# Optimization experiments

Measured on AMD Instinct MI355X. Metric: run time of the kernel, lower is better.

The kernel has to match this reference:

```python
import jax, jax.numpy as jnp
import numpy as np

B, C, H, W = 8, 256, 128, 128
CQ = C // 8


def setup_inputs() -> dict:
    key = jax.random.key(0)
    ks = jax.random.split(key, 8)
    s = 1.0 / np.sqrt(C)
    return {
        "x": jax.random.normal(ks[0], (B, C, H, W), dtype=jnp.float32),
        "wq": jax.random.normal(ks[1], (CQ, C), dtype=jnp.float32) * s,
        "bq": jax.random.normal(ks[2], (CQ,), dtype=jnp.float32) * 0.01,
        "wk": jax.random.normal(ks[3], (CQ, C), dtype=jnp.float32) * s,
        "bk": jax.random.normal(ks[4], (CQ,), dtype=jnp.float32) * 0.01,
        "wv": jax.random.normal(ks[5], (C, C), dtype=jnp.float32) * s,
        "bv": jax.random.normal(ks[6], (C,), dtype=jnp.float32) * 0.01,
        "gamma": jax.random.normal(ks[7], (1,), dtype=jnp.float32) * 0.1,
    }


def reference(x, wq, bq, wk, bk, wv, bv, gamma):
    b, c, h, w = x.shape
    # 1x1 convs == channel matmuls
    q = jnp.einsum("oc,bchw->bohw", wq, x) + bq[None, :, None, None]  # [B,Cq,H,W]
    k = jnp.einsum("oc,bchw->bohw", wk, x) + bk[None, :, None, None]  # [B,Cq,H,W]
    v = jnp.einsum("oc,bchw->bohw", wv, x) + bv[None, :, None, None]  # [B,C,H,W]

    # column (height) scores: energy_H[b,i,w,j] = <k[:, i, w], q[:, j, w]>, -inf on i==j
    e_h = jnp.einsum("bciw,bcjw->biwj", k, q)  # [B,H,W,H]
    diag = jnp.eye(h, dtype=bool)[:, None, :]  # [H,1,H] -> masks i==j
    e_h = jnp.where(diag[None], -jnp.inf, e_h)

    # row (width) scores: energy_W[b,h,i,j] = <k[:, h, i], q[:, h, j]>
    e_w = jnp.einsum("bchi,bchj->bhij", k, q)  # [B,H,W,W]

    # joint softmax over concatenated H+W scores (axis 3), as in the torch code
    att = jax.nn.softmax(jnp.concatenate([e_h, e_w], axis=3), axis=3)
    a_h, a_w = att[..., :h], att[..., h:]

    out_h = jnp.einsum("bciw,biwj->bcjw", v, a_h)  # aggregate along column
    out_w = jnp.einsum("bchi,bhij->bchj", v, a_w)  # aggregate along row
    return gamma * (out_h + out_w) + x
```

## Files before the change

kernel.cpp:

```cpp
#include <hip/hip_runtime.h>
#include <math.h>

#define C_   256
#define CQ_  32
#define H_   128
#define W_   128
#define HW_  (H_ * W_)
#define OC_  320

typedef __attribute__((ext_vector_type(8))) short  s8v;
typedef __attribute__((ext_vector_type(4))) float  f4v;
typedef __attribute__((ext_vector_type(8))) unsigned short u8v;
typedef __attribute__((ext_vector_type(4))) unsigned short u4v;

__device__ inline unsigned short f2bf(float f) {
    unsigned int u = __float_as_uint(f);
    unsigned int r = (u + 0x7fffu + ((u >> 16) & 1u)) >> 16;
    return (unsigned short)r;
}
__device__ inline float bfu(unsigned short u) {
    return __uint_as_float((unsigned int)u << 16);
}

__global__ __launch_bounds__(256) void k_wconv(
    const float* __restrict__ wq, const float* __restrict__ wk,
    const float* __restrict__ wv, unsigned short* __restrict__ Wb)
{
    int idx4 = blockIdx.x * 256 + threadIdx.x;
    int e = idx4 * 4;
    int oc = e >> 8, k = e & 255;
    const float* src;
    if (oc < 32)      src = wq + (size_t)oc * C_ + k;
    else if (oc < 64) src = wk + (size_t)(oc - 32) * C_ + k;
    else              src = wv + (size_t)(oc - 64) * C_ + k;
    float4 v = *(const float4*)src;
    u4v o;
    o[0] = f2bf(v.x); o[1] = f2bf(v.y); o[2] = f2bf(v.z); o[3] = f2bf(v.w);
    *(u4v*)(Wb + e) = o;
}

__global__ __launch_bounds__(256) void k_qkv(
    const float* __restrict__ x, const unsigned short* __restrict__ Wb,
    const float* __restrict__ bq, const float* __restrict__ bk,
    const float* __restrict__ bv,
    unsigned short* __restrict__ qkv, int b0)
{
    __shared__ __align__(16) unsigned short Wl[2][64][72];
    __shared__ __align__(16) unsigned int   Xp[2][32 * 132];
    const int t = threadIdx.x;
    const int lane = t & 63;
    const int wave = t >> 6;
    const int n0 = blockIdx.x * 128;
    const int ocblk = blockIdx.y * 64;
    const int bb = blockIdx.z;
    const float* xb = x + (size_t)(b0 + bb) * C_ * HW_;

    const int lg = lane >> 4;
    const int ll = lane & 15;
    const int n_w = wave * 32;

    const int kp8 = t >> 5;
    const int n4  = (t & 31) * 4;
    const int wrow = t >> 3;
    const int wcg  = (t & 7) * 8;
    float4 ra[4], rb[4];
    u8v wreg[2];

    #pragma unroll
    for (int p = 0; p < 4; ++p) {
        int krow = (p * 8 + kp8) * 2;
        ra[p] = *(const float4*)(xb + (size_t)krow * HW_ + n0 + n4);
        rb[p] = *(const float4*)(xb + (size_t)(krow + 1) * HW_ + n0 + n4);
    }
    #pragma unroll
    for (int q = 0; q < 2; ++q)
        wreg[q] = *(const u8v*)(Wb + (size_t)(ocblk + wrow + q * 32) * C_ + wcg);

    #pragma unroll
    for (int p = 0; p < 4; ++p) {
        uint4 d;
        const float* af  = (const float*)&ra[p];
        const float* bf_ = (const float*)&rb[p];
        #pragma unroll
        for (int i = 0; i < 4; ++i) {
            unsigned int lo = (__float_as_uint(af[i])  + 0x8000u) >> 16;
            unsigned int hi = (__float_as_uint(bf_[i]) + 0x8000u) & 0xffff0000u;
            ((unsigned int*)&d)[i] = hi | lo;
        }
        *(uint4*)&Xp[0][(p * 8 + kp8) * 132 + n4] = d;
    }
    #pragma unroll
    for (int q = 0; q < 2; ++q)
        *(u8v*)&Wl[0][wrow + q * 32][wcg] = wreg[q];

    #pragma unroll
    for (int p = 0; p < 4; ++p) {
        int krow = 64 + (p * 8 + kp8) * 2;
        ra[p] = *(const float4*)(xb + (size_t)krow * HW_ + n0 + n4);
        rb[p] = *(const float4*)(xb + (size_t)(krow + 1) * HW_ + n0 + n4);
    }
    #pragma unroll
    for (int q = 0; q < 2; ++q)
        wreg[q] = *(const u8v*)(Wb + (size_t)(ocblk + wrow + q * 32) * C_ + 64 + wcg);

    f4v acc[4][2];
    #pragma unroll
    for (int mr = 0; mr < 4; ++mr)
        #pragma unroll
        for (int nr = 0; nr < 2; ++nr)
            acc[mr][nr] = (f4v){0.f, 0.f, 0.f, 0.f};

    __syncthreads();

    #pragma unroll
    for (int kc = 0; kc < 4; ++kc) {
        const int cur = kc & 1;
        if (kc < 3) {
            #pragma unroll
            for (int p = 0; p < 4; ++p) {
                uint4 d;
                const float* af  = (const float*)&ra[p];
                const float* bf_ = (const float*)&rb[p];
                #pragma unroll
                for (int i = 0; i < 4; ++i) {
                    unsigned int lo = (__float_as_uint(af[i])  + 0x8000u) >> 16;
                    unsigned int hi = (__float_as_uint(bf_[i]) + 0x8000u) & 0xffff0000u;
                    ((unsigned int*)&d)[i] = hi | lo;
                }
                *(uint4*)&Xp[cur ^ 1][(p * 8 + kp8) * 132 + n4] = d;
            }
            #pragma unroll
            for (int q = 0; q < 2; ++q)
                *(u8v*)&Wl[cur ^ 1][wrow + q * 32][wcg] = wreg[q];
        }
        if (kc < 2) {
            #pragma unroll
            for (int p = 0; p < 4; ++p) {
                int krow = (kc + 2) * 64 + (p * 8 + kp8) * 2;
                ra[p] = *(const float4*)(xb + (size_t)krow * HW_ + n0 + n4);
                rb[p] = *(const float4*)(xb + (size_t)(krow + 1) * HW_ + n0 + n4);
            }
            #pragma unroll
            for (int q = 0; q < 2; ++q)
                wreg[q] = *(const u8v*)(
                    Wb + (size_t)(ocblk + wrow + q * 32) * C_ + (kc + 2) * 64 + wcg);
        }
        #pragma unroll
        for (int ks = 0; ks < 2; ++ks) {
            s8v afr[4];
            #pragma unroll
            for (int mr = 0; mr < 4; ++mr)
                afr[mr] = *(const s8v*)&Wl[cur][mr * 16 + ll][ks * 32 + lg * 8];
            #pragma unroll
            for (int nr = 0; nr < 2; ++nr) {
                int4 bd;
                #pragma unroll
                for (int e2 = 0; e2 < 4; ++e2)
                    ((int*)&bd)[e2] =
                        Xp[cur][(ks * 16 + lg * 4 + e2) * 132 + n_w + nr * 16 + ll];
                s8v bfr = *(s8v*)&bd;
                #pragma unroll
                for (int mr = 0; mr < 4; ++mr)
                    acc[mr][nr] = __builtin_amdgcn_mfma_f32_16x16x32_bf16(
                        afr[mr], bfr, acc[mr][nr], 0, 0, 0);
            }
        }
        __syncthreads();
    }

    #pragma unroll
    for (int mr = 0; mr < 4; ++mr) {
        float bias[4];
        #pragma unroll
        for (int r = 0; r < 4; ++r) {
            int oc = ocblk + mr * 16 + lg * 4 + r;
            if (oc < 32)      bias[r] = bq[oc];
            else if (oc < 64) bias[r] = bk[oc - 32];
            else              bias[r] = bv[oc - 64];
        }
        #pragma unroll
        for (int nr = 0; nr < 2; ++nr) {
            int n = n0 + n_w + nr * 16 + ll;
            #pragma unroll
            for (int r = 0; r < 4; ++r) {
                int oc = ocblk + mr * 16 + lg * 4 + r;
                qkv[((size_t)bb * OC_ + oc) * HW_ + n] = f2bf(acc[mr][nr][r] + bias[r]);
            }
        }
    }
}

__global__ __launch_bounds__(256) void k_transpose_qkv(
    const unsigned short* __restrict__ qkv, unsigned short* __restrict__ qkv_t)
{
    __shared__ unsigned short tile[32][34];
    const int bb = blockIdx.z;
    const int oc = blockIdx.y;
    const int th = (blockIdx.x & 3) * 32;
    const int tw = (blockIdx.x >> 2) * 32;
    const unsigned short* src = qkv + ((size_t)bb * OC_ + oc) * HW_;
    #pragma unroll
    for (int r = 0; r < 4; ++r) {
        int h = threadIdx.y * 4 + r;
        tile[h][threadIdx.x] = src[(size_t)(th + h) * W_ + tw + threadIdx.x];
    }
    __syncthreads();
    unsigned short* dst = qkv_t + (size_t)bb * W_ * OC_ * H_;
    #pragma unroll
    for (int r = 0; r < 4; ++r) {
        int wl = threadIdx.y * 4 + r;
        dst[((size_t)(tw + wl) * OC_ + oc) * H_ + th + threadIdx.x] = tile[threadIdx.x][wl];
    }
}

__device__ inline void stage_KQ(const unsigned short* base, int cstride,
                                unsigned int* Ktp, unsigned int* Qp, int t)
{
    {
        int i = t & 127, half = t >> 7, c0 = half * 16;
        unsigned int kr[16];
        #pragma unroll
        for (int cc = 0; cc < 16; ++cc)
            kr[cc] = base[(size_t)(32 + c0 + cc) * cstride + i];
        uint4 d0, d1;
        #pragma unroll
        for (int e2 = 0; e2 < 4; ++e2)
            ((unsigned int*)&d0)[e2] = kr[2 * e2] | (kr[2 * e2 + 1] << 16);
        #pragma unroll
        for (int e2 = 0; e2 < 4; ++e2)
            ((unsigned int*)&d1)[e2] = kr[8 + 2 * e2] | (kr[9 + 2 * e2] << 16);
        *(uint4*)&Ktp[i * 20 + half * 8]     = d0;
        *(uint4*)&Ktp[i * 20 + half * 8 + 4] = d1;
    }
    {
        int c2 = t >> 4, j8 = (t & 15) * 8;
        u8v qa = *(const u8v*)(base + (size_t)(2 * c2) * cstride + j8);
        u8v qb = *(const u8v*)(base + (size_t)(2 * c2 + 1) * cstride + j8);
        uint4 e0, e1;
        #pragma unroll
        for (int e = 0; e < 4; ++e)
            ((unsigned int*)&e0)[e] =
                (unsigned int)qa[e] | ((unsigned int)qb[e] << 16);
        #pragma unroll
        for (int e = 0; e < 4; ++e)
            ((unsigned int*)&e1)[e] =
                (unsigned int)qa[4 + e] | ((unsigned int)qb[4 + e] << 16);
        *(uint4*)&Qp[c2 * 132 + j8]     = e0;
        *(uint4*)&Qp[c2 * 132 + j8 + 4] = e1;
    }
}

__device__ inline f4v eqk_mfma(const unsigned int* Ktp, const unsigned int* Qp,
                               int mr, int j, int lg, int ll)
{
    s8v afr = *(const s8v*)&Ktp[(mr * 16 + ll) * 20 + lg * 4];
    int4 bd;
    #pragma unroll
    for (int e2 = 0; e2 < 4; ++e2)
        ((int*)&bd)[e2] = Qp[(lg * 4 + e2) * 132 + j];
    s8v bfr = *(s8v*)&bd;
    return __builtin_amdgcn_mfma_f32_16x16x32_bf16(
        afr, bfr, (f4v){0.f, 0.f, 0.f, 0.f}, 0, 0, 0);
}

__global__ __launch_bounds__(256) void k_stats_h(
    const unsigned short* __restrict__ qkv_t,
    float* __restrict__ mh, float* __restrict__ sh)
{
    __shared__ __align__(16) unsigned int Ktp[128 * 20];
    __shared__ __align__(16) unsigned int Qp[16 * 132];
    const int t = threadIdx.x;
    const int beta = blockIdx.x;
    const int bb = blockIdx.y;
    const unsigned short* base = qkv_t + ((size_t)bb * W_ + beta) * OC_ * H_;
    stage_KQ(base, H_, Ktp, Qp, t);
    __syncthreads();

    const int lane = t & 63;
    const int wv = t >> 6;
    const int lg = lane >> 4;
    const int ll = lane & 15;

    #pragma unroll
    for (int ml = 0; ml < 2; ++ml) {
        const int mr = wv * 2 + ml;
        const int i0 = mr * 16 + lg * 4;
        f4v ef[8];
        #pragma unroll
        for (int nt = 0; nt < 8; ++nt) {
            f4v e = eqk_mfma(Ktp, Qp, mr, nt * 16 + ll, lg, ll);
            int j = nt * 16 + ll;
            #pragma unroll
            for (int r = 0; r < 4; ++r)
                if (i0 + r == j) e[r] = -INFINITY;
            ef[nt] = e;
        }
        #pragma unroll
        for (int r = 0; r < 4; ++r) {
            float mm = -INFINITY;
            #pragma unroll
            for (int nt = 0; nt < 8; ++nt) mm = fmaxf(mm, ef[nt][r]);
            #pragma unroll
            for (int s = 1; s < 16; s <<= 1) mm = fmaxf(mm, __shfl_xor(mm, s));
            float ss = 0.f;
            #pragma unroll
            for (int nt = 0; nt < 8; ++nt) ss += __expf(ef[nt][r] - mm);
            #pragma unroll
            for (int s = 1; s < 16; s <<= 1) ss += __shfl_xor(ss, s);
            if (ll == 0) {
                int i = i0 + r;
                mh[((size_t)bb * H_ + i) * W_ + beta] = mm;
                sh[((size_t)bb * H_ + i) * W_ + beta] = ss;
            }
        }
    }
}

__global__ __launch_bounds__(256) void k_stats_w(
    const unsigned short* __restrict__ qkv,
    float* __restrict__ mw, float* __restrict__ sw)
{
    __shared__ __align__(16) unsigned int Ktp[128 * 20];
    __shared__ __align__(16) unsigned int Qp[16 * 132];
    const int t = threadIdx.x;
    const int alpha = blockIdx.x;
    const int bb = blockIdx.y;
    const unsigned short* base = qkv + (size_t)bb * OC_ * HW_ + (size_t)alpha * W_;
    stage_KQ(base, HW_, Ktp, Qp, t);
    __syncthreads();

    const int lane = t & 63;
    const int wv = t >> 6;
    const int lg = lane >> 4;
    const int ll = lane & 15;

    #pragma unroll
    for (int ml = 0; ml < 2; ++ml) {
        const int mr = wv * 2 + ml;
        const int i0 = mr * 16 + lg * 4;
        f4v ef[8];
        #pragma unroll
        for (int nt = 0; nt < 8; ++nt)
            ef[nt] = eqk_mfma(Ktp, Qp, mr, nt * 16 + ll, lg, ll);
        #pragma unroll
        for (int r = 0; r < 4; ++r) {
            float mm = -INFINITY;
            #pragma unroll
            for (int nt = 0; nt < 8; ++nt) mm = fmaxf(mm, ef[nt][r]);
            #pragma unroll
            for (int s = 1; s < 16; s <<= 1) mm = fmaxf(mm, __shfl_xor(mm, s));
            float ss = 0.f;
            #pragma unroll
            for (int nt = 0; nt < 8; ++nt) ss += __expf(ef[nt][r] - mm);
            #pragma unroll
            for (int s = 1; s < 16; s <<= 1) ss += __shfl_xor(ss, s);
            if (ll == 0) {
                int i = i0 + r;
                mw[((size_t)bb * H_ + alpha) * W_ + i] = mm;
                sw[((size_t)bb * H_ + alpha) * W_ + i] = ss;
            }
        }
    }
}

__global__ __launch_bounds__(256) void k_prep(
    const float* __restrict__ mh, const float* __restrict__ sh,
    const float* __restrict__ mw, const float* __restrict__ sw,
    float* __restrict__ mc, float* __restrict__ dv,
    float* __restrict__ mct, float* __restrict__ dvt, int n)
{
    int idx = blockIdx.x * 256 + threadIdx.x;
    if (idx >= n) return;
    float m1 = mh[idx], s1 = sh[idx], m2 = mw[idx], s2 = sw[idx];
    float m = fmaxf(m1, m2);
    float d = 1.f / (s1 * __expf(m1 - m) + s2 * __expf(m2 - m));
    mc[idx] = m; dv[idx] = d;
    int q = idx & (W_ - 1);
    int p = (idx >> 7) & (H_ - 1);
    int b = idx >> 14;
    size_t tid = ((size_t)b * W_ + q) * H_ + p;
    mct[tid] = m; dvt[tid] = d;
}

__global__ __launch_bounds__(256) void k_outh(
    const unsigned short* __restrict__ qkv_t,
    const float* __restrict__ mct, const float* __restrict__ dvt,
    unsigned short* __restrict__ oh_t)
{
    __shared__ __align__(16) unsigned short Pt[128 * 128];
    __shared__ __align__(16) unsigned char  Ubuf[18688];
    __shared__ float mloc[128], dloc[128];
    unsigned int* Ktp = (unsigned int*)Ubuf;
    unsigned int* Qp  = (unsigned int*)(Ubuf + 10240);
    unsigned short* Vl = (unsigned short*)Ubuf;

    const int t = threadIdx.x;
    const int beta = blockIdx.x;
    const int bb = blockIdx.y;
    const unsigned short* base = qkv_t + ((size_t)bb * W_ + beta) * OC_ * H_;

    if (t < 128) {
        size_t sidx = ((size_t)bb * W_ + beta) * H_ + t;
        mloc[t] = mct[sidx];
        dloc[t] = dvt[sidx];
    }
    stage_KQ(base, H_, Ktp, Qp, t);

    const int vc  = t >> 4;
    const int vi0 = (t & 15) * 8;
    u8v vreg[4];
    {
        const unsigned short* vsrc = base + (size_t)64 * H_;
        #pragma unroll
        for (int q = 0; q < 4; ++q)
            vreg[q] = *(const u8v*)(vsrc + (size_t)(vc + q * 16) * H_ + vi0);
    }
    __syncthreads();

    const int lane = t & 63;
    const int wv = t >> 6;
    const int lg = lane >> 4;
    const int ll = lane & 15;
    const int jq0 = wv * 32;

    #pragma unroll
    for (int mr = 0; mr < 8; ++mr) {
        const int i0 = mr * 16 + lg * 4;
        float mi[4], di[4];
        #pragma unroll
        for (int r = 0; r < 4; ++r) { mi[r] = mloc[i0 + r]; di[r] = dloc[i0 + r]; }
        #pragma unroll
        for (int nt = 0; nt < 2; ++nt) {
            int j = jq0 + nt * 16 + ll;
            f4v e = eqk_mfma(Ktp, Qp, mr, j, lg, ll);
            float p0 = (i0     == j) ? 0.f : __expf(e[0] - mi[0]) * di[0];
            float p1 = (i0 + 1 == j) ? 0.f : __expf(e[1] - mi[1]) * di[1];
            float p2 = (i0 + 2 == j) ? 0.f : __expf(e[2] - mi[2]) * di[2];
            float p3 = (i0 + 3 == j) ? 0.f : __expf(e[3] - mi[3]) * di[3];
            uint2 wd;
            wd.x = f2bf(p0) | ((unsigned int)f2bf(p1) << 16);
            wd.y = f2bf(p2) | ((unsigned int)f2bf(p3) << 16);
            int sidx = (j * 128 + i0) ^ ((j & 7) << 3);
            *(uint2*)&Pt[sidx] = wd;
        }
    }

    unsigned short* outbase = oh_t + ((size_t)bb * W_ + beta) * C_ * H_;
    const int cw = (wv & 1) * 32;
    const int jw = (wv >> 1) * 64;

    for (int ch = 0; ch < 4; ++ch) {
        __syncthreads();
        #pragma unroll
        for (int q = 0; q < 4; ++q) {
            int c = vc + q * 16;
            *(u8v*)&Vl[(c * 128 + vi0) ^ ((c & 7) << 3)] = vreg[q];
        }
        __syncthreads();
        if (ch < 3) {
            const unsigned short* vsrc = base + (size_t)(64 + (ch + 1) * 64) * H_;
            #pragma unroll
            for (int q = 0; q < 4; ++q)
                vreg[q] = *(const u8v*)(vsrc + (size_t)(vc + q * 16) * H_ + vi0);
        }

        f4v acc[2][4];
        #pragma unroll
        for (int cr = 0; cr < 2; ++cr)
            #pragma unroll
            for (int nt = 0; nt < 4; ++nt)
                acc[cr][nt] = (f4v){0.f, 0.f, 0.f, 0.f};

        #pragma unroll
        for (int kk = 0; kk < 4; ++kk) {
            s8v afr[2];
            #pragma unroll
            for (int cr = 0; cr < 2; ++cr) {
                int crow = cw + cr * 16 + ll;
                afr[cr] = *(const s8v*)&Vl[(crow * 128 + kk * 32 + lg * 8) ^ ((crow & 7) << 3)];
            }
            #pragma unroll
            for (int nt = 0; nt < 4; ++nt) {
                int j = jw + nt * 16 + ll;
                s8v bfr = *(const s8v*)&Pt[(j * 128 + kk * 32 + lg * 8) ^ ((j & 7) << 3)];
                acc[0][nt] = __builtin_amdgcn_mfma_f32_16x16x32_bf16(afr[0], bfr, acc[0][nt], 0, 0, 0);
                acc[1][nt] = __builtin_amdgcn_mfma_f32_16x16x32_bf16(afr[1], bfr, acc[1][nt], 0, 0, 0);
            }
        }
        #pragma unroll
        for (int cr = 0; cr < 2; ++cr)
            #pragma unroll
            for (int nt = 0; nt < 4; ++nt) {
                int j = jw + nt * 16 + ll;
                #pragma unroll
                for (int r = 0; r < 4; ++r) {
                    int c = ch * 64 + cw + cr * 16 + lg * 4 + r;
                    outbase[(size_t)c * H_ + j] = f2bf(acc[cr][nt][r]);
                }
            }
    }
}

__global__ __launch_bounds__(256) void k_outw(
    const unsigned short* __restrict__ qkv,
    const float* __restrict__ mc, const float* __restrict__ dv_,
    unsigned short* __restrict__ ow)
{
    __shared__ __align__(16) unsigned short Pt[128 * 128];
    __shared__ __align__(16) unsigned char  Ubuf[18688];
    __shared__ float mloc[128], dloc[128];
    unsigned int* Ktp = (unsigned int*)Ubuf;
    unsigned int* Qp  = (unsigned int*)(Ubuf + 10240);
    unsigned short* Vl = (unsigned short*)Ubuf;

    const int t = threadIdx.x;
    const int alpha = blockIdx.x;
    const int bb = blockIdx.y;
    const unsigned short* base = qkv + (size_t)bb * OC_ * HW_ + (size_t)alpha * W_;

    if (t < 128) {
        size_t sidx = ((size_t)bb * H_ + alpha) * W_ + t;
        mloc[t] = mc[sidx];
        dloc[t] = dv_[sidx];
    }
    stage_KQ(base, HW_, Ktp, Qp, t);

    const int vc  = t >> 4;
    const int vi0 = (t & 15) * 8;
    u8v vreg[4];
    {
        const unsigned short* vsrc = base + (size_t)64 * HW_;
        #pragma unroll
        for (int q = 0; q < 4; ++q)
            vreg[q] = *(const u8v*)(vsrc + (size_t)(vc + q * 16) * HW_ + vi0);
    }
    __syncthreads();

    const int lane = t & 63;
    const int wv = t >> 6;
    const int lg = lane >> 4;
    const int ll = lane & 15;
    const int jq0 = wv * 32;

    #pragma unroll
    for (int mr = 0; mr < 8; ++mr) {
        const int i0 = mr * 16 + lg * 4;
        float mi[4], di[4];
        #pragma unroll
        for (int r = 0; r < 4; ++r) { mi[r] = mloc[i0 + r]; di[r] = dloc[i0 + r]; }
        #pragma unroll
        for (int nt = 0; nt < 2; ++nt) {
            int j = jq0 + nt * 16 + ll;
            f4v e = eqk_mfma(Ktp, Qp, mr, j, lg, ll);
            float p0 = __expf(e[0] - mi[0]) * di[0];
            float p1 = __expf(e[1] - mi[1]) * di[1];
            float p2 = __expf(e[2] - mi[2]) * di[2];
            float p3 = __expf(e[3] - mi[3]) * di[3];
            uint2 wd;
            wd.x = f2bf(p0) | ((unsigned int)f2bf(p1) << 16);
            wd.y = f2bf(p2) | ((unsigned int)f2bf(p3) << 16);
            int sidx = (j * 128 + i0) ^ ((j & 7) << 3);
            *(uint2*)&Pt[sidx] = wd;
        }
    }

    unsigned short* obase = ow + (size_t)bb * C_ * HW_ + (size_t)alpha * W_;
    const int cw = (wv & 1) * 32;
    const int jw = (wv >> 1) * 64;

    for (int ch = 0; ch < 4; ++ch) {
        __syncthreads();
        #pragma unroll
        for (int q = 0; q < 4; ++q) {
            int c = vc + q * 16;
            *(u8v*)&Vl[(c * 128 + vi0) ^ ((c & 7) << 3)] = vreg[q];
        }
        __syncthreads();
        if (ch < 3) {
            const unsigned short* vsrc = base + (size_t)(64 + (ch + 1) * 64) * HW_;
            #pragma unroll
            for (int q = 0; q < 4; ++q)
                vreg[q] = *(const u8v*)(vsrc + (size_t)(vc + q * 16) * HW_ + vi0);
        }

        f4v acc[2][4];
        #pragma unroll
        for (int cr = 0; cr < 2; ++cr)
            #pragma unroll
            for (int nt = 0; nt < 4; ++nt)
                acc[cr][nt] = (f4v){0.f, 0.f, 0.f, 0.f};

        #pragma unroll
        for (int kk = 0; kk < 4; ++kk) {
            s8v afr[2];
            #pragma unroll
            for (int cr = 0; cr < 2; ++cr) {
                int crow = cw + cr * 16 + ll;
                afr[cr] = *(const s8v*)&Vl[(crow * 128 + kk * 32 + lg * 8) ^ ((crow & 7) << 3)];
            }
            #pragma unroll
            for (int nt = 0; nt < 4; ++nt) {
                int j = jw + nt * 16 + ll;
                s8v bfr = *(const s8v*)&Pt[(j * 128 + kk * 32 + lg * 8) ^ ((j & 7) << 3)];
                acc[0][nt] = __builtin_amdgcn_mfma_f32_16x16x32_bf16(afr[0], bfr, acc[0][nt], 0, 0, 0);
                acc[1][nt] = __builtin_amdgcn_mfma_f32_16x16x32_bf16(afr[1], bfr, acc[1][nt], 0, 0, 0);
            }
        }
        #pragma unroll
        for (int cr = 0; cr < 2; ++cr)
            #pragma unroll
            for (int nt = 0; nt < 4; ++nt) {
                int j = jw + nt * 16 + ll;
                #pragma unroll
                for (int r = 0; r < 4; ++r) {
                    int c = ch * 64 + cw + cr * 16 + lg * 4 + r;
                    obase[(size_t)c * HW_ + j] = f2bf(acc[cr][nt][r]);
                }
            }
    }
}

__global__ __launch_bounds__(256) void k_combine(
    const unsigned short* __restrict__ oh_t, const unsigned short* __restrict__ ow,
    const float* __restrict__ x, const float* __restrict__ gamma_p,
    float* __restrict__ out, int b0)
{
    __shared__ float tile[32][33];
    const int bb = blockIdx.z;
    const int c = blockIdx.y;
    const int th = (blockIdx.x & 3) * 32;
    const int tw = (blockIdx.x >> 2) * 32;
    const float gamma = gamma_p[0];
    const unsigned short* src = oh_t + (size_t)bb * W_ * C_ * H_;
    #pragma unroll
    for (int r = 0; r < 4; ++r) {
        int wl = threadIdx.y * 4 + r;
        tile[wl][threadIdx.x] =
            bfu(src[((size_t)(tw + wl) * C_ + c) * H_ + th + threadIdx.x]);
    }
    __syncthreads();
    const size_t pbase = ((size_t)bb * C_ + c) * HW_;
    const size_t gbase = ((size_t)(b0 + bb) * C_ + c) * HW_;
    #pragma unroll
    for (int r = 0; r < 4; ++r) {
        int hl = threadIdx.y * 4 + r;
        size_t idx = (size_t)(th + hl) * W_ + tw + threadIdx.x;
        float owv = bfu(ow[pbase + idx]);
        out[gbase + idx] = x[gbase + idx] + gamma * (owv + tile[threadIdx.x][hl]);
    }
}

extern "C" void kernel_launch(void* const* d_in, const int* in_sizes, int n_in,
                              void* d_out, int out_size, void* d_ws, size_t ws_size,
                              hipStream_t stream)
{
    (void)in_sizes; (void)n_in; (void)out_size;
    const float* x  = (const float*)d_in[0];
    const float* wq = (const float*)d_in[1];
    const float* bq = (const float*)d_in[2];
    const float* wk = (const float*)d_in[3];
    const float* bk = (const float*)d_in[4];
    const float* wv = (const float*)d_in[5];
    const float* bv = (const float*)d_in[6];
    const float* gm = (const float*)d_in[7];
    float* out = (float*)d_out;

    const size_t e_qkv  = (size_t)OC_ * HW_;
    const size_t e_out  = (size_t)C_ * HW_;
    const size_t e_stat = (size_t)HW_;
    const size_t perb_bytes = (e_qkv * 2 + e_out * 2) * 2 + e_stat * 8 * 4;
    const size_t wb_bytes = (size_t)OC_ * C_ * 2;
    int nbcap = (int)((ws_size - wb_bytes) / perb_bytes);
    if (nbcap > 8) nbcap = 8;
    if (nbcap < 1) nbcap = 1;

    unsigned short* Wb    = (unsigned short*)d_ws;
    unsigned short* qkv   = Wb    + (size_t)OC_ * C_;
    unsigned short* qkv_t = qkv   + e_qkv * nbcap;
    unsigned short* oh    = qkv_t + e_qkv * nbcap;
    unsigned short* ow    = oh    + e_out * nbcap;
    float* mh  = (float*)(ow + e_out * nbcap);
    float* sh  = mh  + e_stat * nbcap;
    float* mw  = sh  + e_stat * nbcap;
    float* sw  = mw  + e_stat * nbcap;
    float* mc  = sw  + e_stat * nbcap;
    float* dv  = mc  + e_stat * nbcap;
    float* mct = dv  + e_stat * nbcap;
    float* dvt = mct + e_stat * nbcap;

    k_wconv<<<dim3(80), 256, 0, stream>>>(wq, wk, wv, Wb);

    for (int b0 = 0; b0 < 8; b0 += nbcap) {
        int nb = 8 - b0 < nbcap ? 8 - b0 : nbcap;
        k_qkv<<<dim3(HW_ / 128, 5, nb), 256, 0, stream>>>(
            x, Wb, bq, bk, bv, qkv, b0);
        k_transpose_qkv<<<dim3(16, OC_, nb), dim3(32, 8), 0, stream>>>(qkv, qkv_t);
        k_stats_h<<<dim3(W_, nb), 256, 0, stream>>>(qkv_t, mh, sh);
        k_stats_w<<<dim3(H_, nb), 256, 0, stream>>>(qkv, mw, sw);
        int nstat = nb * HW_;
        k_prep<<<dim3((nstat + 255) / 256), 256, 0, stream>>>(
            mh, sh, mw, sw, mc, dv, mct, dvt, nstat);
        k_outh<<<dim3(W_, nb), 256, 0, stream>>>(qkv_t, mct, dvt, oh);
        k_outw<<<dim3(H_, nb), 256, 0, stream>>>(qkv, mc, dv, ow);
        k_combine<<<dim3(16, C_, nb), dim3(32, 8), 0, stream>>>(
            oh, ow, x, gm, out, b0);
    }
}
```

Measured before the change: 289.9 us.

## Pre-pack x and weights into MFMA fragment layout, drop LDS staging in QKV GEMM

Adds a k_xconv pass that converts x to bf16 and stores it in a fragment-major layout matching the 16x16x32 MFMA operand order. The weight conversion kernel writes weights in the same packed layout. k_qkv then loads A and B fragments straight from global memory into registers with a 3-deep register pipeline, with no LDS tiles or barriers. This removes the LDS staging and syncs, but adds an extra launch plus a bf16 write and read of x. Each weight fragment is also reread from global/L2 by every block instead of being shared through LDS.

```diff
diff --git a/kernel.cpp b/kernel.cpp
--- a/kernel.cpp
+++ b/kernel.cpp
@@ -24,84 +24,78 @@
 
 __global__ __launch_bounds__(256) void k_wconv(
     const float* __restrict__ wq, const float* __restrict__ wk,
-    const float* __restrict__ wv, unsigned short* __restrict__ Wb)
-{
-    int idx4 = blockIdx.x * 256 + threadIdx.x;
-    int e = idx4 * 4;
-    int oc = e >> 8, k = e & 255;
-    const float* src;
-    if (oc < 32)      src = wq + (size_t)oc * C_ + k;
-    else if (oc < 64) src = wk + (size_t)(oc - 32) * C_ + k;
-    else              src = wv + (size_t)(oc - 64) * C_ + k;
-    float4 v = *(const float4*)src;
-    u4v o;
-    o[0] = f2bf(v.x); o[1] = f2bf(v.y); o[2] = f2bf(v.z); o[3] = f2bf(v.w);
-    *(u4v*)(Wb + e) = o;
+    const float* __restrict__ wv, unsigned short* __restrict__ wF)
+{
+    int u = blockIdx.x * 256 + threadIdx.x;
+    int ocg = u >> 9;
+    int ll  = u & 15;
+    int k0  = ((u >> 4) & 31) * 8;
+    int oc  = ocg * 16 + ll;
+    const float* row;
+    if (oc < 32)      row = wq + (size_t)oc * C_;
+    else if (oc < 64) row = wk + (size_t)(oc - 32) * C_;
+    else              row = wv + (size_t)(oc - 64) * C_;
+    unsigned short o[8];
+    #pragma unroll
+    for (int e = 0; e < 8; ++e) o[e] = f2bf(row[k0 + e]);
+    *(u8v*)(wF + (size_t)u * 8) = *(u8v*)o;
+}
+
+__global__ __launch_bounds__(256) void k_xconv(
+    const float* __restrict__ x, unsigned short* __restrict__ xF, int b0)
+{
+    __shared__ float tile[32][33];
+    const int t  = threadIdx.x;
+    const int n0 = (blockIdx.x & 511) * 32;
+    const int c0 = (blockIdx.x >> 9) * 32;
+    const int bb = blockIdx.y;
+    const float* src = x + ((size_t)(b0 + bb) * C_ + c0) * HW_ + n0;
+    const int tx = t & 31, ty = t >> 5;
+    #pragma unroll
+    for (int r = 0; r < 4; ++r)
+        tile[ty * 4 + r][tx] = src[(size_t)(ty * 4 + r) * HW_ + tx];
+    __syncthreads();
+    if (t < 128) {
+        const int nl = t & 31, kg = t >> 5;
+        unsigned short o[8];
+        #pragma unroll
+        for (int e = 0; e < 8; ++e) o[e] = f2bf(tile[kg * 8 + e][nl]);
+        const size_t g = (size_t)((n0 + nl) >> 4);
+        unsigned short* dst = xF + (size_t)bb * C_ * HW_
+            + ((g * 32 + (c0 >> 3) + kg) * 16 + ((n0 + nl) & 15)) * 8;
+        *(u8v*)dst = *(u8v*)o;
+    }
 }
 
 __global__ __launch_bounds__(256) void k_qkv(
-    const float* __restrict__ x, const unsigned short* __restrict__ Wb,
+    const unsigned short* __restrict__ xF, const unsigned short* __restrict__ wF,
     const float* __restrict__ bq, const float* __restrict__ bk,
-    const float* __restrict__ bv,
-    unsigned short* __restrict__ qkv, int b0)
-{
-    __shared__ __align__(16) unsigned short Wl[2][64][72];
-    __shared__ __align__(16) unsigned int   Xp[2][32 * 132];
+    const float* __restrict__ bv, unsigned short* __restrict__ qkv)
+{
     const int t = threadIdx.x;
     const int lane = t & 63;
     const int wave = t >> 6;
     const int n0 = blockIdx.x * 128;
     const int ocblk = blockIdx.y * 64;
     const int bb = blockIdx.z;
-    const float* xb = x + (size_t)(b0 + bb) * C_ * HW_;
-
     const int lg = lane >> 4;
     const int ll = lane & 15;
     const int n_w = wave * 32;
 
-    const int kp8 = t >> 5;
-    const int n4  = (t & 31) * 4;
-    const int wrow = t >> 3;
-    const int wcg  = (t & 7) * 8;
-    float4 ra[4], rb[4];
-    u8v wreg[2];
-
-    #pragma unroll
-    for (int p = 0; p < 4; ++p) {
-        int krow = (p * 8 + kp8) * 2;
-        ra[p] = *(const float4*)(xb + (size_t)krow * HW_ + n0 + n4);
-        rb[p] = *(const float4*)(xb + (size_t)(krow + 1) * HW_ + n0 + n4);
-    }
-    #pragma unroll
-    for (int q = 0; q < 2; ++q)
-        wreg[q] = *(const u8v*)(Wb + (size_t)(ocblk + wrow + q * 32) * C_ + wcg);
-
-    #pragma unroll
-    for (int p = 0; p < 4; ++p) {
-        uint4 d;
-        const float* af  = (const float*)&ra[p];
-        const float* bf_ = (const float*)&rb[p];
-        #pragma unroll
-        for (int i = 0; i < 4; ++i) {
-            unsigned int lo = (__float_as_uint(af[i])  + 0x8000u) >> 16;
-            unsigned int hi = (__float_as_uint(bf_[i]) + 0x8000u) & 0xffff0000u;
-            ((unsigned int*)&d)[i] = hi | lo;
-        }
-        *(uint4*)&Xp[0][(p * 8 + kp8) * 132 + n4] = d;
-    }
-    #pragma unroll
-    for (int q = 0; q < 2; ++q)
-        *(u8v*)&Wl[0][wrow + q * 32][wcg] = wreg[q];
-
-    #pragma unroll
-    for (int p = 0; p < 4; ++p) {
-        int krow = 64 + (p * 8 + kp8) * 2;
-        ra[p] = *(const float4*)(xb + (size_t)krow * HW_ + n0 + n4);
-        rb[p] = *(const float4*)(xb + (size_t)(krow + 1) * HW_ + n0 + n4);
-    }
-    #pragma unroll
-    for (int q = 0; q < 2; ++q)
-        wreg[q] = *(const u8v*)(Wb + (size_t)(ocblk + wrow + q * 32) * C_ + 64 + wcg);
+    const unsigned short* Bb = xF + (size_t)bb * C_ * HW_
+        + (((size_t)((n0 >> 4) + wave * 2) * 32 + lg) * 16 + ll) * 8;
+    const unsigned short* Ab = wF
+        + (((size_t)(ocblk >> 4) * 32 + lg) * 16 + ll) * 8;
+
+    s8v Af[3][4];
+    s8v Bf[3][2];
+#define LOADSTEP(buf, s)                                          \
+    Af[buf][0] = *(const s8v*)(Ab + (s) * 512 +     0);           \
+    Af[buf][1] = *(const s8v*)(Ab + (s) * 512 +  4096);           \
+    Af[buf][2] = *(const s8v*)(Ab + (s) * 512 +  8192);           \
+    Af[buf][3] = *(const s8v*)(Ab + (s) * 512 + 12288);           \
+    Bf[buf][0] = *(const s8v*)(Bb + (s) * 512 +     0);           \
+    Bf[buf][1] = *(const s8v*)(Bb + (s) * 512 +  4096);
 
     f4v acc[4][2];
     #pragma unroll
@@ -110,63 +104,23 @@
         for (int nr = 0; nr < 2; ++nr)
             acc[mr][nr] = (f4v){0.f, 0.f, 0.f, 0.f};
 
-    __syncthreads();
-
-    #pragma unroll
-    for (int kc = 0; kc < 4; ++kc) {
-        const int cur = kc & 1;
-        if (kc < 3) {
-            #pragma unroll
-            for (int p = 0; p < 4; ++p) {
-                uint4 d;
-                const float* af  = (const float*)&ra[p];
-                const float* bf_ = (const float*)&rb[p];
-                #pragma unroll
-                for (int i = 0; i < 4; ++i) {
-                    unsigned int lo = (__float_as_uint(af[i])  + 0x8000u) >> 16;
-                    unsigned int hi = (__float_as_uint(bf_[i]) + 0x8000u) & 0xffff0000u;
-                    ((unsigned int*)&d)[i] = hi | lo;
-                }
-                *(uint4*)&Xp[cur ^ 1][(p * 8 + kp8) * 132 + n4] = d;
-            }
-            #pragma unroll
-            for (int q = 0; q < 2; ++q)
-                *(u8v*)&Wl[cur ^ 1][wrow + q * 32][wcg] = wreg[q];
-        }
-        if (kc < 2) {
-            #pragma unroll
-            for (int p = 0; p < 4; ++p) {
-                int krow = (kc + 2) * 64 + (p * 8 + kp8) * 2;
-                ra[p] = *(const float4*)(xb + (size_t)krow * HW_ + n0 + n4);
-                rb[p] = *(const float4*)(xb + (size_t)(krow + 1) * HW_ + n0 + n4);
-            }
-            #pragma unroll
-            for (int q = 0; q < 2; ++q)
-                wreg[q] = *(const u8v*)(
-                    Wb + (size_t)(ocblk + wrow + q * 32) * C_ + (kc + 2) * 64 + wcg);
-        }
-        #pragma unroll
-        for (int ks = 0; ks < 2; ++ks) {
-            s8v afr[4];
+    LOADSTEP(0, 0)
+    LOADSTEP(1, 1)
+    #pragma unroll
+    for (int s = 0; s < 8; ++s) {
+        const int cur = s % 3;
+        if (s < 6) {
+            const int nxt = (s + 2) % 3;
+            LOADSTEP(nxt, s + 2)
+        }
+        #pragma unroll
+        for (int nr = 0; nr < 2; ++nr)
             #pragma unroll
             for (int mr = 0; mr < 4; ++mr)
-                afr[mr] = *(const s8v*)&Wl[cur][mr * 16 + ll][ks * 32 + lg * 8];
-            #pragma unroll
-            for (int nr = 0; nr < 2; ++nr) {
-                int4 bd;
-                #pragma unroll
-                for (int e2 = 0; e2 < 4; ++e2)
-                    ((int*)&bd)[e2] =
-                        Xp[cur][(ks * 16 + lg * 4 + e2) * 132 + n_w + nr * 16 + ll];
-                s8v bfr = *(s8v*)&bd;
-                #pragma unroll
-                for (int mr = 0; mr < 4; ++mr)
-                    acc[mr][nr] = __builtin_amdgcn_mfma_f32_16x16x32_bf16(
-                        afr[mr], bfr, acc[mr][nr], 0, 0, 0);
-            }
-        }
-        __syncthreads();
-    }
+                acc[mr][nr] = __builtin_amdgcn_mfma_f32_16x16x32_bf16(
+                    Af[cur][mr], Bf[cur][nr], acc[mr][nr], 0, 0, 0);
+    }
+#undef LOADSTEP
 
     #pragma unroll
     for (int mr = 0; mr < 4; ++mr) {
@@ -667,19 +621,21 @@
 
     const size_t e_qkv  = (size_t)OC_ * HW_;
     const size_t e_out  = (size_t)C_ * HW_;
+    const size_t e_x    = (size_t)C_ * HW_;
     const size_t e_stat = (size_t)HW_;
-    const size_t perb_bytes = (e_qkv * 2 + e_out * 2) * 2 + e_stat * 8 * 4;
+    const size_t perb_bytes = (e_qkv * 2 + e_out * 2 + e_x) * 2 + e_stat * 8 * 4;
     const size_t wb_bytes = (size_t)OC_ * C_ * 2;
     int nbcap = (int)((ws_size - wb_bytes) / perb_bytes);
     if (nbcap > 8) nbcap = 8;
     if (nbcap < 1) nbcap = 1;
 
-    unsigned short* Wb    = (unsigned short*)d_ws;
-    unsigned short* qkv   = Wb    + (size_t)OC_ * C_;
+    unsigned short* wF    = (unsigned short*)d_ws;
+    unsigned short* qkv   = wF    + (size_t)OC_ * C_;
     unsigned short* qkv_t = qkv   + e_qkv * nbcap;
     unsigned short* oh    = qkv_t + e_qkv * nbcap;
     unsigned short* ow    = oh    + e_out * nbcap;
-    float* mh  = (float*)(ow + e_out * nbcap);
+    unsigned short* xF    = ow    + e_out * nbcap;
+    float* mh  = (float*)(xF + e_x * nbcap);
     float* sh  = mh  + e_stat * nbcap;
     float* mw  = sh  + e_stat * nbcap;
     float* sw  = mw  + e_stat * nbcap;
@@ -688,12 +644,13 @@
     float* mct = dv  + e_stat * nbcap;
     float* dvt = mct + e_stat * nbcap;
 
-    k_wconv<<<dim3(80), 256, 0, stream>>>(wq, wk, wv, Wb);
+    k_wconv<<<dim3(40), 256, 0, stream>>>(wq, wk, wv, wF);
 
     for (int b0 = 0; b0 < 8; b0 += nbcap) {
         int nb = 8 - b0 < nbcap ? 8 - b0 : nbcap;
+        k_xconv<<<dim3((HW_ / 32) * (C_ / 32), nb), 256, 0, stream>>>(x, xF, b0);
         k_qkv<<<dim3(HW_ / 128, 5, nb), 256, 0, stream>>>(
-            x, Wb, bq, bk, bv, qkv, b0);
+            xF, wF, bq, bk, bv, qkv);
         k_transpose_qkv<<<dim3(16, OC_, nb), dim3(32, 8), 0, stream>>>(qkv, qkv_t);
         k_stats_h<<<dim3(W_, nb), 256, 0, stream>>>(qkv_t, mh, sh);
         k_stats_w<<<dim3(H_, nb), 256, 0, stream>>>(qkv, mw, sw);
```

Result: slower. 306.3 us (median of 2 runs) (+5.6%).
